# Kernel tuning notes

Measured on AMD Instinct MI355X. Metric: run time of the kernel, lower is better.

The kernel has to match this reference:

```python
import jax, jax.numpy as jnp
import numpy as np

EPS = 1e-8
INL_TH = 2.0          # RANSAC inl_th default; oneway_transfer_error squared=True
MIN_SAMPLE = 4        # minimal_sample_size for homography
MAX_LO_ITERS = 5      # RANSAC max_lo_iters
DLT_ITERS = 5         # find_homography_dlt_iterated n_iter default
SOFT_INL_TH = 3.0     # find_homography_dlt_iterated soft_inl_th default


def normalize_points(pts):
    # pts: (B,N,2) -> normalized points + (B,3,3) transforms (kornia normalize_points)
    mean = pts.mean(axis=1, keepdims=True)                      # (B,1,2)
    scale = jnp.linalg.norm(pts - mean, axis=-1).mean(axis=-1)  # (B,)
    scale = jnp.asarray(np.sqrt(2.0), pts.dtype) / (scale + EPS)
    pts_n = (pts - mean) * scale[:, None, None]
    mx, my = mean[:, 0, 0], mean[:, 0, 1]
    z = jnp.zeros_like(scale)
    o = jnp.ones_like(scale)
    T = jnp.stack([scale, z, -scale * mx,
                   z, scale, -scale * my,
                   z, z, o], axis=-1).reshape(-1, 3, 3)
    return pts_n, T


def find_homography_dlt(p1, p2, w):
    # weighted normalized DLT: p1,p2 (B,N,2), w (B,N) -> H (B,3,3)
    B = p1.shape[0]
    p1n, T1 = normalize_points(p1)
    p2n, T2 = normalize_points(p2)
    x1, y1 = p1n[..., 0], p1n[..., 1]
    x2, y2 = p2n[..., 0], p2n[..., 1]
    o = jnp.ones_like(x1)
    z = jnp.zeros_like(x1)
    ax = jnp.stack([z, z, z, -x1, -y1, -o, y2 * x1, y2 * y1, y2], axis=-1)  # (B,N,9)
    ay = jnp.stack([x1, y1, o, z, z, z, -x2 * x1, -x2 * y1, -x2], axis=-1)  # (B,N,9)
    A = jnp.stack([ax, ay], axis=2).reshape(B, -1, 9)   # (B,2N,9), ax/ay rows interleaved
    w2 = jnp.repeat(w, 2, axis=1)                       # repeat_interleave to match rows
    AtA = jnp.einsum('bni,bn,bnj->bij', A, w2, A)       # (B,9,9)
    _, _, Vh = jnp.linalg.svd(AtA)
    H = Vh[:, -1].reshape(-1, 3, 3)                     # null vector
    H = jnp.linalg.inv(T2) @ H @ T1                     # denormalize
    return H / (H[:, 2:3, 2:3] + EPS)


def transfer_errors(H, p1, p2, squared=True):
    # oneway_transfer_error: H (B,3,3), p1,p2 (N,2) -> (B,N)
    p1h = jnp.concatenate([p1, jnp.ones_like(p1[..., :1])], axis=-1)  # (N,3)
    proj = jnp.einsum('bij,nj->bni', H, p1h)                          # (B,N,3)
    zc = proj[..., 2:3]
    s = jnp.where(jnp.abs(zc) > EPS, 1.0 / zc, jnp.ones_like(zc))
    pt = proj[..., :2] * s
    err = ((pt - p2) ** 2).sum(-1)
    return err if squared else jnp.sqrt(jnp.maximum(err, 0.0))


def sample_is_valid_for_homography(p1, p2):
    # orientation-consistency of 4-point minimal samples: (B,4,2) -> (B,)
    trip = jnp.array([[0, 1, 2], [0, 2, 3], [0, 1, 3], [1, 2, 3]])
    p1h = jnp.concatenate([p1, jnp.ones_like(p1[..., :1])], axis=-1)
    p2h = jnp.concatenate([p2, jnp.ones_like(p2[..., :1])], axis=-1)
    d1 = jnp.linalg.det(p1h[:, trip])  # (B,4) triple-product signs
    d2 = jnp.linalg.det(p2h[:, trip])
    return jnp.all(jnp.sign(d1) == jnp.sign(d2), axis=1)


def polish_model(kp1, kp2, inl_mask):
    # find_homography_dlt_iterated; inlier subset expressed as zero/one weights
    w = inl_mask.astype(kp1.dtype)[None]  # (1,N)
    p1, p2 = kp1[None], kp2[None]
    H = find_homography_dlt(p1, p2, w)
    for _ in range(DLT_ITERS - 1):
        err = transfer_errors(H, kp1, kp2, squared=False)
        w_new = jnp.exp(-err / (2.0 * SOFT_INL_TH ** 2))
        H = find_homography_dlt(p1, p2, w * w_new)
    return H


def ransac_forward(kp1, kp2, idxs):
    dtype = kp1.dtype
    N = kp1.shape[0]
    kp1s, kp2s = kp1[idxs], kp2[idxs]  # (B,4,2) minimal samples
    valid_sample = sample_is_valid_for_homography(kp1s, kp2s)  # remove_bad_samples (as score mask)
    w = jnp.ones(kp1s.shape[:2], dtype)
    models = find_homography_dlt(kp1s, kp2s, w)                # (B,3,3)
    diag_min = jnp.abs(jnp.diagonal(models, axis1=1, axis2=2)).min(axis=1)
    valid_model = diag_min > 1e-4                              # remove_bad_models (as score mask)
    errors = transfer_errors(models, kp1, kp2)                 # (B,N) verify
    inl = errors <= INL_TH
    scores = inl.astype(dtype).sum(axis=1)
    scores = jnp.where(valid_sample & valid_model, scores, jnp.asarray(-1.0, dtype))
    best = jnp.argmax(scores)
    model, inliers, score = models[best], inl[best], scores[best]
    accept = score > float(MIN_SAMPLE)  # best_score_total init = minimal_sample_size

    def lo_body(carry, _):
        m, il, sc = carry
        m_lo = polish_model(kp1, kp2, il)           # (1,3,3)
        err_lo = transfer_errors(m_lo, kp1, kp2)[0]
        il_lo = err_lo <= INL_TH
        sc_lo = il_lo.astype(dtype).sum()
        better = sc_lo > sc                         # non-improving step is a fixed point == break
        m = jnp.where(better, m_lo[0], m)
        il = jnp.where(better, il_lo, il)
        sc = jnp.where(better, sc_lo, sc)
        return (m, il, sc), None

    (model, inliers, score), _ = jax.lax.scan(lo_body, (model, inliers, score), None, length=MAX_LO_ITERS)
    best_model = jnp.where(accept, model, jnp.zeros((3, 3), dtype))
    best_inliers = jnp.where(accept, inliers, jnp.zeros((N,), bool))
    return best_model, best_inliers


def setup_inputs():
    key = jax.random.key(0)
    k1, k2, k3, k4, k5 = jax.random.split(key, 5)
    N, B = 10000, 2048
    kp1 = jax.random.uniform(k1, (N, 2), jnp.float32) * 1000.0
    H_gt = jnp.array([[1.02, 0.01, 10.0], [-0.02, 0.98, -5.0], [1e-5, -1e-5, 1.0]], jnp.float32)
    p1h = jnp.concatenate([kp1, jnp.ones((N, 1), jnp.float32)], axis=-1)
    proj = p1h @ H_gt.T
    proj = proj[:, :2] / proj[:, 2:3]
    noise = jax.random.normal(k2, (N, 2), jnp.float32) * 0.5
    outliers = jax.random.uniform(k3, (N, 2), jnp.float32) * 1000.0
    is_out = jax.random.uniform(k4, (N,)) < 0.5
    kp2 = jnp.where(is_out[:, None], outliers, proj + noise)
    # minimal-sample indices without replacement (torch: rand.topk(k=4, dim=1))
    rand = jax.random.uniform(k5, (B, N))
    _, idxs = jax.lax.top_k(rand, 4)
    return {"kp1": kp1, "kp2": kp2, "idxs": idxs}


def reference(kp1, kp2, idxs):
    return ransac_forward(kp1, kp2, idxs)
```

## Files before the change

### kernel.cpp

```cpp
#include <hip/hip_runtime.h>
#include <math.h>


struct Hdr {
  int best_idx;
  float best_score;
  int pad0, pad1;
  double nrm[6];
};

__device__ __forceinline__ float sq_err9(const float h[9], float x1, float y1,
                                         float x2, float y2) {
  float px = h[0] * x1 + h[1] * y1 + h[2];
  float py = h[3] * x1 + h[4] * y1 + h[5];
  float pz = h[6] * x1 + h[7] * y1 + h[8];
  float s  = (fabsf(pz) > 1e-8f) ? (1.0f / pz) : 1.0f;
  float dx = px * s - x2;
  float dy = py * s - y2;
  return dx * dx + dy * dy;
}

__device__ __forceinline__ constexpr int TIDX(int i, int j) {
  return i * 9 - i * (i - 1) / 2 + (j - i);
}

__device__ __forceinline__ void accum_packed_f32(float* ata, float w, float x1,
                                                 float y1, float x2, float y2) {
  const int ia[6] = {3, 4, 5, 6, 7, 8};
  const int ib[6] = {0, 1, 2, 6, 7, 8};
  float va[6] = {-x1, -y1, -1.0f, x1 * y2, y1 * y2, y2};
  float vb[6] = {x1, y1, 1.0f, -x1 * x2, -y1 * x2, -x2};
#pragma unroll
  for (int u = 0; u < 6; u++) {
    float wa = w * va[u];
#pragma unroll
    for (int v = u; v < 6; v++) ata[TIDX(ia[u], ia[v])] += wa * va[v];
  }
#pragma unroll
  for (int u = 0; u < 6; u++) {
    float wb = w * vb[u];
#pragma unroll
    for (int v = u; v < 6; v++) ata[TIDX(ib[u], ib[v])] += wb * vb[v];
  }
}

__device__ __forceinline__ void accum_full_f64(double M[9][9], double x1,
                                               double y1, double x2, double y2) {
  const int ia[6] = {3, 4, 5, 6, 7, 8};
  const int ib[6] = {0, 1, 2, 6, 7, 8};
  double va[6] = {-x1, -y1, -1.0, x1 * y2, y1 * y2, y2};
  double vb[6] = {x1, y1, 1.0, -x1 * x2, -y1 * x2, -x2};
#pragma unroll
  for (int u = 0; u < 6; u++)
#pragma unroll
    for (int v = u; v < 6; v++) M[ia[u]][ia[v]] += va[u] * va[v];
#pragma unroll
  for (int u = 0; u < 6; u++)
#pragma unroll
    for (int v = u; v < 6; v++) M[ib[u]][ib[v]] += vb[u] * vb[v];
}

__device__ __forceinline__ void solve_null9(double M[9][9], double h[9]) {
  double tr = 0.0;
#pragma unroll
  for (int i = 0; i < 9; i++) {
    tr += M[i][i];
#pragma unroll
    for (int j = i + 1; j < 9; j++) M[j][i] = M[i][j];
  }
  double ridge = tr * 1e-12 + 1e-30;
#pragma unroll
  for (int i = 0; i < 9; i++) M[i][i] += ridge;
#pragma unroll
  for (int j = 0; j < 9; j++) {
    double d = M[j][j];
#pragma unroll
    for (int k = 0; k < j; k++) d -= M[j][k] * M[j][k];
    d = (d > 1e-280) ? d : 1e-280;
    double dj = sqrt(d);
    M[j][j] = dj;
    double inv = 1.0 / dj;
#pragma unroll
    for (int i = j + 1; i < 9; i++) {
      double v = M[i][j];
#pragma unroll
      for (int k = 0; k < j; k++) v -= M[i][k] * M[j][k];
      M[i][j] = v * inv;
    }
  }
  double x[9] = {1, 1, 1, 1, 1, 1, 1, 1, 1};
#pragma unroll
  for (int it = 0; it < 3; ++it) {
#pragma unroll
    for (int i = 0; i < 9; i++) {
      double v = x[i];
#pragma unroll
      for (int k = 0; k < i; k++) v -= M[i][k] * x[k];
      x[i] = v / M[i][i];
    }
#pragma unroll
    for (int i = 8; i >= 0; i--) {
      double v = x[i];
#pragma unroll
      for (int k = i + 1; k < 9; k++) v -= M[k][i] * x[k];
      x[i] = v / M[i][i];
    }
    double mx = fabs(x[0]);
#pragma unroll
    for (int i = 1; i < 9; i++) mx = fmax(mx, fabs(x[i]));
    double r = 1.0 / mx;
#pragma unroll
    for (int i = 0; i < 9; i++) x[i] *= r;
  }
#pragma unroll
  for (int i = 0; i < 9; i++) h[i] = x[i];
}

__device__ __forceinline__ void denorm9(const double hh[9], double mx1,
                                        double my1, double s1, double mx2,
                                        double my2, double s2, float out[9]) {
  double is2 = 1.0 / s2;
  double g0 = is2 * hh[0] + mx2 * hh[6];
  double g1 = is2 * hh[1] + mx2 * hh[7];
  double g2 = is2 * hh[2] + mx2 * hh[8];
  double g3 = is2 * hh[3] + my2 * hh[6];
  double g4 = is2 * hh[4] + my2 * hh[7];
  double g5 = is2 * hh[5] + my2 * hh[8];
  double g6 = hh[6], g7 = hh[7], g8 = hh[8];
  double a = -s1 * mx1, b = -s1 * my1;
  double H0 = s1 * g0, H1 = s1 * g1, H2 = a * g0 + b * g1 + g2;
  double H3 = s1 * g3, H4 = s1 * g4, H5 = a * g3 + b * g4 + g5;
  double H6 = s1 * g6, H7 = s1 * g7, H8 = a * g6 + b * g7 + g8;
  double inv = 1.0 / (H8 + 1e-8);
  out[0] = (float)(H0 * inv);
  out[1] = (float)(H1 * inv);
  out[2] = (float)(H2 * inv);
  out[3] = (float)(H3 * inv);
  out[4] = (float)(H4 * inv);
  out[5] = (float)(H5 * inv);
  out[6] = (float)(H6 * inv);
  out[7] = (float)(H7 * inv);
  out[8] = (float)(H8 * inv);
}

__global__ __launch_bounds__(256, 2) void k_fit_score(
    const float2* __restrict__ kp1, const float2* __restrict__ kp2,
    const int* __restrict__ idxs, int N, float* __restrict__ models,
    float* __restrict__ scores) {
  __shared__ float sH[9];
  __shared__ int sValid;
  __shared__ int sCnt[4];
  const int b = blockIdx.x;
  const int t = threadIdx.x;

  if (t == 0) {
    double X1[4], Y1[4], X2[4], Y2[4];
#pragma unroll
    for (int k = 0; k < 4; k++) {
      int id = idxs[b * 4 + k];
      float2 a = kp1[id];
      float2 c = kp2[id];
      X1[k] = a.x; Y1[k] = a.y; X2[k] = c.x; Y2[k] = c.y;
    }
    const int t0[4] = {0, 0, 0, 1};
    const int t1[4] = {1, 2, 1, 2};
    const int t2[4] = {2, 3, 3, 3};
    bool vs = true;
#pragma unroll
    for (int q = 0; q < 4; q++) {
      int i0 = t0[q], i1 = t1[q], i2 = t2[q];
      double d1 = (X1[i1] - X1[i0]) * (Y1[i2] - Y1[i0]) -
                  (X1[i2] - X1[i0]) * (Y1[i1] - Y1[i0]);
      double d2 = (X2[i1] - X2[i0]) * (Y2[i2] - Y2[i0]) -
                  (X2[i2] - X2[i0]) * (Y2[i1] - Y2[i0]);
      int sg1 = (d1 > 0.0) ? 1 : ((d1 < 0.0) ? -1 : 0);
      int sg2 = (d2 > 0.0) ? 1 : ((d2 < 0.0) ? -1 : 0);
      vs = vs && (sg1 == sg2);
    }
    double mx1 = (X1[0] + X1[1] + X1[2] + X1[3]) * 0.25;
    double my1 = (Y1[0] + Y1[1] + Y1[2] + Y1[3]) * 0.25;
    double mx2 = (X2[0] + X2[1] + X2[2] + X2[3]) * 0.25;
    double my2 = (Y2[0] + Y2[1] + Y2[2] + Y2[3]) * 0.25;
    double n1 = 0.0, n2 = 0.0;
#pragma unroll
    for (int k = 0; k < 4; k++) {
      double dx = X1[k] - mx1, dy = Y1[k] - my1;
      n1 += sqrt(dx * dx + dy * dy);
      dx = X2[k] - mx2; dy = Y2[k] - my2;
      n2 += sqrt(dx * dx + dy * dy);
    }
    double s1 = sqrt(2.0) / (n1 * 0.25 + 1e-8);
    double s2 = sqrt(2.0) / (n2 * 0.25 + 1e-8);
    double M[9][9];
#pragma unroll
    for (int i = 0; i < 9; i++)
#pragma unroll
      for (int j = 0; j < 9; j++) M[i][j] = 0.0;
#pragma unroll
    for (int k = 0; k < 4; k++)
      accum_full_f64(M, (X1[k] - mx1) * s1, (Y1[k] - my1) * s1,
                     (X2[k] - mx2) * s2, (Y2[k] - my2) * s2);
    double hh[9];
    solve_null9(M, hh);
    float Hf[9];
    denorm9(hh, mx1, my1, s1, mx2, my2, s2, Hf);
    bool vm =
        fminf(fminf(fabsf(Hf[0]), fabsf(Hf[4])), fabsf(Hf[8])) > 1e-4f;
#pragma unroll
    for (int j = 0; j < 9; j++) sH[j] = Hf[j];
    sValid = (vs && vm) ? 1 : 0;
  }
  __syncthreads();

  float h[9];
#pragma unroll
  for (int j = 0; j < 9; j++) h[j] = sH[j];
  int cnt = 0;
  for (int i = t; i < N; i += 256) {
    float2 a = kp1[i];
    float2 c = kp2[i];
    cnt += (sq_err9(h, a.x, a.y, c.x, c.y) <= 2.0f) ? 1 : 0;
  }
#pragma unroll
  for (int off = 32; off; off >>= 1) cnt += __shfl_down(cnt, off);
  if ((t & 63) == 0) sCnt[t >> 6] = cnt;
  __syncthreads();
  if (t == 0) {
    int tot = sCnt[0] + sCnt[1] + sCnt[2] + sCnt[3];
    scores[b] = sValid ? (float)tot : -1.0f;
#pragma unroll
    for (int j = 0; j < 9; j++) models[b * 9 + j] = sH[j];
  }
}

__global__ __launch_bounds__(1024) void k_select(
    const float2* __restrict__ kp1, const float2* __restrict__ kp2, int N,
    int B, const float* __restrict__ scores, Hdr* __restrict__ hdr) {
  const int t = threadIdx.x;
  const int lane = t & 63, wid = t >> 6;
  __shared__ float rs[1024];
  __shared__ int ri[1024];

  float bs = -2.0f;
  int bi = 0x7fffffff;
  for (int i = t; i < B; i += 1024) {
    float s = scores[i];
    if (s > bs || (s == bs && i < bi)) { bs = s; bi = i; }
  }
  rs[t] = bs;
  ri[t] = bi;
  __syncthreads();
  for (int off = 512; off; off >>= 1) {
    if (t < off) {
      float s = rs[t + off];
      int i2 = ri[t + off];
      if (s > rs[t] || (s == rs[t] && i2 < ri[t])) { rs[t] = s; ri[t] = i2; }
    }
    __syncthreads();
  }
  if (t == 0) {
    hdr->best_idx = ri[0];
    hdr->best_score = rs[0];
  }

  __shared__ double red[16][4];
  __shared__ double mb[4];
  double sx1 = 0, sy1 = 0, sx2 = 0, sy2 = 0;
  for (int i = t; i < N; i += 1024) {
    float2 a = kp1[i];
    float2 c = kp2[i];
    sx1 += a.x; sy1 += a.y; sx2 += c.x; sy2 += c.y;
  }
#pragma unroll
  for (int off = 32; off; off >>= 1) {
    sx1 += __shfl_down(sx1, off);
    sy1 += __shfl_down(sy1, off);
    sx2 += __shfl_down(sx2, off);
    sy2 += __shfl_down(sy2, off);
  }
  if (lane == 0) {
    red[wid][0] = sx1; red[wid][1] = sy1; red[wid][2] = sx2; red[wid][3] = sy2;
  }
  __syncthreads();
  if (t == 0) {
    double a = 0, b2 = 0, c = 0, d = 0;
    for (int w2 = 0; w2 < 16; w2++) {
      a += red[w2][0]; b2 += red[w2][1]; c += red[w2][2]; d += red[w2][3];
    }
    mb[0] = a / N; mb[1] = b2 / N; mb[2] = c / N; mb[3] = d / N;
  }
  __syncthreads();
  double mx1 = mb[0], my1 = mb[1], mx2 = mb[2], my2 = mb[3];
  double sn1 = 0, sn2 = 0;
  for (int i = t; i < N; i += 1024) {
    float2 a = kp1[i];
    float2 c = kp2[i];
    double dx = a.x - mx1, dy = a.y - my1;
    sn1 += sqrt(dx * dx + dy * dy);
    dx = c.x - mx2; dy = c.y - my2;
    sn2 += sqrt(dx * dx + dy * dy);
  }
#pragma unroll
  for (int off = 32; off; off >>= 1) {
    sn1 += __shfl_down(sn1, off);
    sn2 += __shfl_down(sn2, off);
  }
  __syncthreads();
  if (lane == 0) { red[wid][0] = sn1; red[wid][1] = sn2; }
  __syncthreads();
  if (t == 0) {
    double a = 0, b2 = 0;
    for (int w2 = 0; w2 < 16; w2++) { a += red[w2][0]; b2 += red[w2][1]; }
    hdr->nrm[0] = mx1;
    hdr->nrm[1] = my1;
    hdr->nrm[2] = sqrt(2.0) / (a / N + 1e-8);
    hdr->nrm[3] = mx2;
    hdr->nrm[4] = my2;
    hdr->nrm[5] = sqrt(2.0) / (b2 / N + 1e-8);
  }
}

#define K3_T 512
#define PPT 20

__global__ __launch_bounds__(512) void k_lo(const float2* __restrict__ kp1,
                                            const float2* __restrict__ kp2,
                                            int N,
                                            const float* __restrict__ models,
                                            const Hdr* __restrict__ hdr,
                                            float* __restrict__ out,
                                            int out_size) {
  const int t = threadIdx.x;
  const int lane = t & 63, wid = t >> 6;
  __shared__ double sAtA[45];
  __shared__ float sWred[8][45];
  __shared__ float sHcur[9];
  __shared__ float sHpol[9];
  __shared__ float sScLo;
  __shared__ int sCnt[8];
  __shared__ double sPar[6];
  __shared__ float sAccept;

  if (t == 0) {
    int bi = hdr->best_idx;
#pragma unroll
    for (int j = 0; j < 9; j++) sHcur[j] = models[bi * 9 + j];
    sAccept = hdr->best_score;
#pragma unroll
    for (int j = 0; j < 6; j++) sPar[j] = hdr->nrm[j];
  }
  __syncthreads();
  const bool accept = sAccept > 4.0f;
  if (!accept) {
    for (int i = t; i < out_size; i += K3_T) out[i] = 0.0f;
    return;
  }
  const float mx1 = (float)sPar[0], my1 = (float)sPar[1], s1 = (float)sPar[2];
  const float mx2 = (float)sPar[3], my2 = (float)sPar[4], s2 = (float)sPar[5];

  float hc[9];
#pragma unroll
  for (int j = 0; j < 9; j++) hc[j] = sHcur[j];
  unsigned int il = 0u;
  for (int p = 0; p < PPT; p++) {
    int i = p * K3_T + t;
    if (i < N) {
      float2 a = kp1[i];
      float2 c = kp2[i];
      if (sq_err9(hc, a.x, a.y, c.x, c.y) <= 2.0f) il |= (1u << p);
    }
  }
  float sc = sAccept;

  for (int lo = 0; lo < 5; ++lo) {
    for (int j = 0; j < 5; ++j) {
      float hp[9];
      if (j > 0) {
#pragma unroll
        for (int q = 0; q < 9; q++) hp[q] = sHpol[q];
      }
      float acc[45];
#pragma unroll
      for (int k = 0; k < 45; k++) acc[k] = 0.0f;
      for (int p = 0; p < PPT; p++) {
        int i = p * K3_T + t;
        if (i < N) {
          float w = ((il >> p) & 1u) ? 1.0f : 0.0f;
          if (w != 0.0f) {
            float2 a = kp1[i];
            float2 c = kp2[i];
            if (j > 0) {
              float e = sq_err9(hp, a.x, a.y, c.x, c.y);
              w = expf(-sqrtf(fmaxf(e, 0.0f)) / 18.0f);
            }
            float xn1 = (a.x - mx1) * s1, yn1 = (a.y - my1) * s1;
            float xn2 = (c.x - mx2) * s2, yn2 = (c.y - my2) * s2;
            accum_packed_f32(acc, w, xn1, yn1, xn2, yn2);
          }
        }
      }
#pragma unroll
      for (int k = 0; k < 45; k++) {
        float v = acc[k];
#pragma unroll
        for (int off = 32; off; off >>= 1) v += __shfl_down(v, off);
        if (lane == 0) sWred[wid][k] = v;
      }
      __syncthreads();
      if (t < 45) {
        double s = 0.0;
#pragma unroll
        for (int w2 = 0; w2 < 8; w2++) s += (double)sWred[w2][t];
        sAtA[t] = s;
      }
      __syncthreads();
      if (t == 0) {
        double M[9][9];
        int k = 0;
#pragma unroll
        for (int i2 = 0; i2 < 9; i2++)
#pragma unroll
          for (int j2 = i2; j2 < 9; j2++) M[i2][j2] = sAtA[k++];
        double hh[9];
        solve_null9(M, hh);
        float ho[9];
        denorm9(hh, sPar[0], sPar[1], sPar[2], sPar[3], sPar[4], sPar[5], ho);
#pragma unroll
        for (int q = 0; q < 9; q++) sHpol[q] = ho[q];
      }
      __syncthreads();
    }
    float hl[9];
#pragma unroll
    for (int q = 0; q < 9; q++) hl[q] = sHpol[q];
    unsigned int il_lo = 0u;
    int cnt = 0;
    for (int p = 0; p < PPT; p++) {
      int i = p * K3_T + t;
      if (i < N) {
        float2 a = kp1[i];
        float2 c = kp2[i];
        if (sq_err9(hl, a.x, a.y, c.x, c.y) <= 2.0f) {
          il_lo |= (1u << p);
          cnt++;
        }
      }
    }
#pragma unroll
    for (int off = 32; off; off >>= 1) cnt += __shfl_down(cnt, off);
    if (lane == 0) sCnt[wid] = cnt;
    __syncthreads();
    if (t == 0) {
      int tot = 0;
#pragma unroll
      for (int w2 = 0; w2 < 8; w2++) tot += sCnt[w2];
      sScLo = (float)tot;
    }
    __syncthreads();
    float sc_lo = sScLo;
    if (sc_lo > sc) {
      il = il_lo;
      sc = sc_lo;
      if (t == 0) {
#pragma unroll
        for (int q = 0; q < 9; q++) sHcur[q] = sHpol[q];
      }
    }
    __syncthreads();
  }

  if (t < 9 && t < out_size) out[t] = sHcur[t];
  for (int p = 0; p < PPT; p++) {
    int i = p * K3_T + t;
    if (i < N && (9 + i) < out_size)
      out[9 + i] = ((il >> p) & 1u) ? 1.0f : 0.0f;
  }
  for (int i = 9 + N + t; i < out_size; i += K3_T) out[i] = 0.0f;
}

extern "C" void kernel_launch(void* const* d_in, const int* in_sizes, int n_in,
                              void* d_out, int out_size, void* d_ws,
                              size_t ws_size, hipStream_t stream) {
  (void)n_in;
  (void)ws_size;
  const float2* kp1 = (const float2*)d_in[0];
  const float2* kp2 = (const float2*)d_in[1];
  const int* idxs = (const int*)d_in[2];
  const int N = in_sizes[0] / 2;
  const int B = in_sizes[2] / 4;

  float* models = (float*)d_ws;
  float* scores = models + (size_t)B * 9;
  size_t off = (((size_t)B * 10 * sizeof(float)) + 15) & ~(size_t)15;
  Hdr* hdr = (Hdr*)((char*)d_ws + off);
  float* outf = (float*)d_out;

  k_fit_score<<<B, 256, 0, stream>>>(kp1, kp2, idxs, N, models, scores);
  k_select<<<1, 1024, 0, stream>>>(kp1, kp2, N, B, scores, hdr);
  k_lo<<<1, K3_T, 0, stream>>>(kp1, kp2, N, models, hdr, outf, out_size);
}
```

Baseline: 682.3 us.

## Parallelize 9x9 null-space solve across a wavefront and restructure reductions

Replaces the single-thread Cholesky/inverse-iteration null-vector solve with a wave-parallel version where each lane holds one matrix row and uses shuffles. The fit kernel now launches one 64-thread wave per sample, builds AtA in parallel from the 8x9 design matrix, and scores with 64 threads instead of 256. The LO kernel splits the 45-entry accumulator into two 21-entry blocks and reduces through shared memory in double instead of 45 shuffle reductions. The cost targeted is the serial single-thread solve latency, which is paid in every fit block and inside the LO loop; in exchange the scoring loop has fewer threads per block and the LO kernel uses a large shared buffer.

```diff
diff --git a/kernel.cpp b/kernel.cpp
--- a/kernel.cpp
+++ b/kernel.cpp
@@ -8,6 +8,10 @@
   int pad0, pad1;
   double nrm[6];
 };
+
+__device__ __host__ constexpr int TRI6(int u, int v) {
+  return u * 6 - u * (u - 1) / 2 + (v - u);
+}
 
 __device__ __forceinline__ float sq_err9(const float h[9], float x1, float y1,
                                          float x2, float y2) {
@@ -20,100 +24,86 @@
   return dx * dx + dy * dy;
 }
 
-__device__ __forceinline__ constexpr int TIDX(int i, int j) {
-  return i * 9 - i * (i - 1) / 2 + (j - i);
-}
-
-__device__ __forceinline__ void accum_packed_f32(float* ata, float w, float x1,
-                                                 float y1, float x2, float y2) {
-  const int ia[6] = {3, 4, 5, 6, 7, 8};
-  const int ib[6] = {0, 1, 2, 6, 7, 8};
-  float va[6] = {-x1, -y1, -1.0f, x1 * y2, y1 * y2, y2};
-  float vb[6] = {x1, y1, 1.0f, -x1 * x2, -y1 * x2, -x2};
-#pragma unroll
-  for (int u = 0; u < 6; u++) {
-    float wa = w * va[u];
-#pragma unroll
-    for (int v = u; v < 6; v++) ata[TIDX(ia[u], ia[v])] += wa * va[v];
-  }
-#pragma unroll
-  for (int u = 0; u < 6; u++) {
-    float wb = w * vb[u];
-#pragma unroll
-    for (int v = u; v < 6; v++) ata[TIDX(ib[u], ib[v])] += wb * vb[v];
-  }
-}
-
-__device__ __forceinline__ void accum_full_f64(double M[9][9], double x1,
-                                               double y1, double x2, double y2) {
-  const int ia[6] = {3, 4, 5, 6, 7, 8};
-  const int ib[6] = {0, 1, 2, 6, 7, 8};
-  double va[6] = {-x1, -y1, -1.0, x1 * y2, y1 * y2, y2};
-  double vb[6] = {x1, y1, 1.0, -x1 * x2, -y1 * x2, -x2};
-#pragma unroll
-  for (int u = 0; u < 6; u++)
-#pragma unroll
-    for (int v = u; v < 6; v++) M[ia[u]][ia[v]] += va[u] * va[v];
-#pragma unroll
-  for (int u = 0; u < 6; u++)
-#pragma unroll
-    for (int v = u; v < 6; v++) M[ib[u]][ib[v]] += vb[u] * vb[v];
-}
-
-__device__ __forceinline__ void solve_null9(double M[9][9], double h[9]) {
-  double tr = 0.0;
-#pragma unroll
-  for (int i = 0; i < 9; i++) {
-    tr += M[i][i];
-#pragma unroll
-    for (int j = i + 1; j < 9; j++) M[j][i] = M[i][j];
-  }
+__device__ __forceinline__ double sel9d(const double* a, int k) {
+  double d = a[0];
+  d = (k == 1) ? a[1] : d;
+  d = (k == 2) ? a[2] : d;
+  d = (k == 3) ? a[3] : d;
+  d = (k == 4) ? a[4] : d;
+  d = (k == 5) ? a[5] : d;
+  d = (k == 6) ? a[6] : d;
+  d = (k == 7) ? a[7] : d;
+  d = (k == 8) ? a[8] : d;
+  return d;
+}
+__device__ __forceinline__ double sel4d(const double* a, int k) {
+  double d = a[0];
+  d = (k == 1) ? a[1] : d;
+  d = (k == 2) ? a[2] : d;
+  d = (k == 3) ? a[3] : d;
+  return d;
+}
+
+__device__ __forceinline__ void wave_solve9(double r[9], int lane, double* xs) {
+  double dself = sel9d(r, lane);
+  double tr = (lane < 9) ? dself : 0.0;
+#pragma unroll
+  for (int m = 1; m <= 8; m <<= 1) tr += __shfl_xor(tr, m);
   double ridge = tr * 1e-12 + 1e-30;
 #pragma unroll
-  for (int i = 0; i < 9; i++) M[i][i] += ridge;
+  for (int k = 0; k < 9; k++)
+    if (lane == k) r[k] += ridge;
+
+  double u[9];
+#pragma unroll
+  for (int k = 0; k < 9; k++) u[k] = 0.0;
+  double invd = 0.0;
+
 #pragma unroll
   for (int j = 0; j < 9; j++) {
-    double d = M[j][j];
-#pragma unroll
-    for (int k = 0; k < j; k++) d -= M[j][k] * M[j][k];
-    d = (d > 1e-280) ? d : 1e-280;
-    double dj = sqrt(d);
-    M[j][j] = dj;
-    double inv = 1.0 / dj;
-#pragma unroll
-    for (int i = j + 1; i < 9; i++) {
-      double v = M[i][j];
-#pragma unroll
-      for (int k = 0; k < j; k++) v -= M[i][k] * M[j][k];
-      M[i][j] = v * inv;
-    }
-  }
-  double x[9] = {1, 1, 1, 1, 1, 1, 1, 1, 1};
+    double dj = __shfl(r[j], j);
+    dj = (dj > 1e-280) ? dj : 1e-280;
+    double is = rsqrt(dj);
+    double s = dj * is;
+    double Lij = r[j] * is;
+    if (lane == j) { Lij = s; invd = is; }
+    r[j] = Lij;
+    double c[9];
+#pragma unroll
+    for (int k = j; k < 9; k++) c[k] = __shfl(r[j], k);
+#pragma unroll
+    for (int k = j; k < 9; k++)
+      if (lane == j) u[k] = c[k];
+    if (lane > j) {
+#pragma unroll
+      for (int k = j + 1; k < 9; k++) r[k] -= Lij * c[k];
+    }
+  }
+
+  double x = 1.0;
 #pragma unroll
   for (int it = 0; it < 3; ++it) {
-#pragma unroll
-    for (int i = 0; i < 9; i++) {
-      double v = x[i];
-#pragma unroll
-      for (int k = 0; k < i; k++) v -= M[i][k] * x[k];
-      x[i] = v / M[i][i];
-    }
-#pragma unroll
-    for (int i = 8; i >= 0; i--) {
-      double v = x[i];
-#pragma unroll
-      for (int k = i + 1; k < 9; k++) v -= M[k][i] * x[k];
-      x[i] = v / M[i][i];
-    }
-    double mx = fabs(x[0]);
-#pragma unroll
-    for (int i = 1; i < 9; i++) mx = fmax(mx, fabs(x[i]));
-    double r = 1.0 / mx;
-#pragma unroll
-    for (int i = 0; i < 9; i++) x[i] *= r;
-  }
-#pragma unroll
-  for (int i = 0; i < 9; i++) h[i] = x[i];
+    double acc = x;
+    double y = 0.0;
+#pragma unroll
+    for (int k = 0; k < 9; k++) {
+      double yk = __shfl(acc * invd, k);
+      if (lane == k) y = yk;
+      if (lane > k) acc -= r[k] * yk;
+    }
+    acc = y;
+#pragma unroll
+    for (int k = 8; k >= 0; k--) {
+      double xk = __shfl(acc * invd, k);
+      if (lane == k) x = xk;
+      if (lane < k) acc -= u[k] * xk;
+    }
+    double m2 = (lane < 9) ? fabs(x) : 0.0;
+#pragma unroll
+    for (int m = 1; m <= 8; m <<= 1) m2 = fmax(m2, __shfl_xor(m2, m));
+    x *= 1.0 / m2;
+  }
+  *xs = x;
 }
 
 __device__ __forceinline__ void denorm9(const double hh[9], double mx1,
@@ -143,72 +133,113 @@
   out[8] = (float)(H8 * inv);
 }
 
-__global__ __launch_bounds__(256, 2) void k_fit_score(
+__device__ __forceinline__ double m_entry(const double* CA, const double* CB,
+                                          int i, int j) {
+  double s = 0.0;
+  if (i >= 3) s += CA[TRI6(i - 3, j - 3)];
+  if ((i < 3 || i >= 6) && (j < 3 || j >= 6)) {
+    int ui = (i < 3) ? i : i - 3;
+    int vj = (j < 3) ? j : j - 3;
+    s += CB[TRI6(ui, vj)];
+  }
+  return s;
+}
+
+__global__ __launch_bounds__(64, 2) void k_fit_score(
     const float2* __restrict__ kp1, const float2* __restrict__ kp2,
     const int* __restrict__ idxs, int N, float* __restrict__ models,
     float* __restrict__ scores) {
+  __shared__ double sA8[8 * 9];
   __shared__ float sH[9];
-  __shared__ int sValid;
-  __shared__ int sCnt[4];
   const int b = blockIdx.x;
-  const int t = threadIdx.x;
-
-  if (t == 0) {
-    double X1[4], Y1[4], X2[4], Y2[4];
-#pragma unroll
-    for (int k = 0; k < 4; k++) {
-      int id = idxs[b * 4 + k];
-      float2 a = kp1[id];
-      float2 c = kp2[id];
-      X1[k] = a.x; Y1[k] = a.y; X2[k] = c.x; Y2[k] = c.y;
-    }
-    const int t0[4] = {0, 0, 0, 1};
-    const int t1[4] = {1, 2, 1, 2};
-    const int t2[4] = {2, 3, 3, 3};
-    bool vs = true;
-#pragma unroll
-    for (int q = 0; q < 4; q++) {
-      int i0 = t0[q], i1 = t1[q], i2 = t2[q];
-      double d1 = (X1[i1] - X1[i0]) * (Y1[i2] - Y1[i0]) -
-                  (X1[i2] - X1[i0]) * (Y1[i1] - Y1[i0]);
-      double d2 = (X2[i1] - X2[i0]) * (Y2[i2] - Y2[i0]) -
-                  (X2[i2] - X2[i0]) * (Y2[i1] - Y2[i0]);
-      int sg1 = (d1 > 0.0) ? 1 : ((d1 < 0.0) ? -1 : 0);
-      int sg2 = (d2 > 0.0) ? 1 : ((d2 < 0.0) ? -1 : 0);
-      vs = vs && (sg1 == sg2);
-    }
-    double mx1 = (X1[0] + X1[1] + X1[2] + X1[3]) * 0.25;
-    double my1 = (Y1[0] + Y1[1] + Y1[2] + Y1[3]) * 0.25;
-    double mx2 = (X2[0] + X2[1] + X2[2] + X2[3]) * 0.25;
-    double my2 = (Y2[0] + Y2[1] + Y2[2] + Y2[3]) * 0.25;
-    double n1 = 0.0, n2 = 0.0;
-#pragma unroll
-    for (int k = 0; k < 4; k++) {
-      double dx = X1[k] - mx1, dy = Y1[k] - my1;
-      n1 += sqrt(dx * dx + dy * dy);
-      dx = X2[k] - mx2; dy = Y2[k] - my2;
-      n2 += sqrt(dx * dx + dy * dy);
-    }
-    double s1 = sqrt(2.0) / (n1 * 0.25 + 1e-8);
-    double s2 = sqrt(2.0) / (n2 * 0.25 + 1e-8);
-    double M[9][9];
-#pragma unroll
-    for (int i = 0; i < 9; i++)
-#pragma unroll
-      for (int j = 0; j < 9; j++) M[i][j] = 0.0;
-#pragma unroll
-    for (int k = 0; k < 4; k++)
-      accum_full_f64(M, (X1[k] - mx1) * s1, (Y1[k] - my1) * s1,
-                     (X2[k] - mx2) * s2, (Y2[k] - my2) * s2);
-    double hh[9];
-    solve_null9(M, hh);
+  const int lane = threadIdx.x;
+
+  double X1[4], Y1[4], X2[4], Y2[4];
+#pragma unroll
+  for (int k = 0; k < 4; k++) {
+    int id = idxs[b * 4 + k];
+    float2 a = kp1[id];
+    float2 c = kp2[id];
+    X1[k] = a.x; Y1[k] = a.y; X2[k] = c.x; Y2[k] = c.y;
+  }
+  const int t0[4] = {0, 0, 0, 1};
+  const int t1[4] = {1, 2, 1, 2};
+  const int t2[4] = {2, 3, 3, 3};
+  bool vs = true;
+#pragma unroll
+  for (int q = 0; q < 4; q++) {
+    int i0 = t0[q], i1 = t1[q], i2 = t2[q];
+    double d1 = (X1[i1] - X1[i0]) * (Y1[i2] - Y1[i0]) -
+                (X1[i2] - X1[i0]) * (Y1[i1] - Y1[i0]);
+    double d2 = (X2[i1] - X2[i0]) * (Y2[i2] - Y2[i0]) -
+                (X2[i2] - X2[i0]) * (Y2[i1] - Y2[i0]);
+    int sg1 = (d1 > 0.0) ? 1 : ((d1 < 0.0) ? -1 : 0);
+    int sg2 = (d2 > 0.0) ? 1 : ((d2 < 0.0) ? -1 : 0);
+    vs = vs && (sg1 == sg2);
+  }
+  double mx1 = (X1[0] + X1[1] + X1[2] + X1[3]) * 0.25;
+  double my1 = (Y1[0] + Y1[1] + Y1[2] + Y1[3]) * 0.25;
+  double mx2 = (X2[0] + X2[1] + X2[2] + X2[3]) * 0.25;
+  double my2 = (Y2[0] + Y2[1] + Y2[2] + Y2[3]) * 0.25;
+  double n1 = 0.0, n2 = 0.0;
+#pragma unroll
+  for (int k = 0; k < 4; k++) {
+    double dx = X1[k] - mx1, dy = Y1[k] - my1;
+    n1 += sqrt(dx * dx + dy * dy);
+    dx = X2[k] - mx2; dy = Y2[k] - my2;
+    n2 += sqrt(dx * dx + dy * dy);
+  }
+  double s1 = sqrt(2.0) / (n1 * 0.25 + 1e-8);
+  double s2 = sqrt(2.0) / (n2 * 0.25 + 1e-8);
+
+  if (lane < 8) {
+    int k = lane >> 1;
+    double xn1 = (sel4d(X1, k) - mx1) * s1;
+    double yn1 = (sel4d(Y1, k) - my1) * s1;
+    double xn2 = (sel4d(X2, k) - mx2) * s2;
+    double yn2 = (sel4d(Y2, k) - my2) * s2;
+    bool odd = (lane & 1) != 0;
+    sA8[lane * 9 + 0] = odd ? xn1 : 0.0;
+    sA8[lane * 9 + 1] = odd ? yn1 : 0.0;
+    sA8[lane * 9 + 2] = odd ? 1.0 : 0.0;
+    sA8[lane * 9 + 3] = odd ? 0.0 : -xn1;
+    sA8[lane * 9 + 4] = odd ? 0.0 : -yn1;
+    sA8[lane * 9 + 5] = odd ? 0.0 : -1.0;
+    sA8[lane * 9 + 6] = odd ? -xn2 * xn1 : yn2 * xn1;
+    sA8[lane * 9 + 7] = odd ? -xn2 * yn1 : yn2 * yn1;
+    sA8[lane * 9 + 8] = odd ? -xn2 : yn2;
+  }
+  __syncthreads();
+
+  double r[9];
+  {
+    int i = (lane < 9) ? lane : 0;
+    double ai[8];
+#pragma unroll
+    for (int l = 0; l < 8; l++) ai[l] = sA8[l * 9 + i];
+#pragma unroll
+    for (int j = 0; j < 9; j++) {
+      double s = 0.0;
+#pragma unroll
+      for (int l = 0; l < 8; l++) s += ai[l] * sA8[l * 9 + j];
+      r[j] = s;
+    }
+  }
+  double xs;
+  wave_solve9(r, lane, &xs);
+
+  double hh[9];
+#pragma unroll
+  for (int k = 0; k < 9; k++) hh[k] = __shfl(xs, k);
+
+  bool valid = vs;
+  if (lane == 0) {
     float Hf[9];
     denorm9(hh, mx1, my1, s1, mx2, my2, s2, Hf);
-    bool vm =
-        fminf(fminf(fabsf(Hf[0]), fabsf(Hf[4])), fabsf(Hf[8])) > 1e-4f;
+    bool vm = fminf(fminf(fabsf(Hf[0]), fabsf(Hf[4])), fabsf(Hf[8])) > 1e-4f;
+    valid = vs && vm;
 #pragma unroll
     for (int j = 0; j < 9; j++) sH[j] = Hf[j];
-    sValid = (vs && vm) ? 1 : 0;
   }
   __syncthreads();
 
@@ -216,18 +247,15 @@
 #pragma unroll
   for (int j = 0; j < 9; j++) h[j] = sH[j];
   int cnt = 0;
-  for (int i = t; i < N; i += 256) {
+  for (int i = lane; i < N; i += 64) {
     float2 a = kp1[i];
     float2 c = kp2[i];
     cnt += (sq_err9(h, a.x, a.y, c.x, c.y) <= 2.0f) ? 1 : 0;
   }
 #pragma unroll
   for (int off = 32; off; off >>= 1) cnt += __shfl_down(cnt, off);
-  if ((t & 63) == 0) sCnt[t >> 6] = cnt;
-  __syncthreads();
-  if (t == 0) {
-    int tot = sCnt[0] + sCnt[1] + sCnt[2] + sCnt[3];
-    scores[b] = sValid ? (float)tot : -1.0f;
+  if (lane == 0) {
+    scores[b] = valid ? (float)cnt : -1.0f;
 #pragma unroll
     for (int j = 0; j < 9; j++) models[b * 9 + j] = sH[j];
   }
@@ -323,17 +351,18 @@
 #define K3_T 512
 #define PPT 20
 
-__global__ __launch_bounds__(512) void k_lo(const float2* __restrict__ kp1,
-                                            const float2* __restrict__ kp2,
-                                            int N,
-                                            const float* __restrict__ models,
-                                            const Hdr* __restrict__ hdr,
-                                            float* __restrict__ out,
-                                            int out_size) {
+__global__ __launch_bounds__(512, 2) void k_lo(const float2* __restrict__ kp1,
+                                               const float2* __restrict__ kp2,
+                                               int N,
+                                               const float* __restrict__ models,
+                                               const Hdr* __restrict__ hdr,
+                                               float* __restrict__ out,
+                                               int out_size) {
   const int t = threadIdx.x;
   const int lane = t & 63, wid = t >> 6;
-  __shared__ double sAtA[45];
-  __shared__ float sWred[8][45];
+  __shared__ float sP[K3_T * 42];
+  __shared__ double sP2[42 * 8];
+  __shared__ double sC[42];
   __shared__ float sHcur[9];
   __shared__ float sHpol[9];
   __shared__ float sScLo;
@@ -379,54 +408,78 @@
 #pragma unroll
         for (int q = 0; q < 9; q++) hp[q] = sHpol[q];
       }
-      float acc[45];
-#pragma unroll
-      for (int k = 0; k < 45; k++) acc[k] = 0.0f;
+      float accA[21], accB[21];
+#pragma unroll
+      for (int k = 0; k < 21; k++) { accA[k] = 0.0f; accB[k] = 0.0f; }
       for (int p = 0; p < PPT; p++) {
         int i = p * K3_T + t;
-        if (i < N) {
-          float w = ((il >> p) & 1u) ? 1.0f : 0.0f;
-          if (w != 0.0f) {
-            float2 a = kp1[i];
-            float2 c = kp2[i];
-            if (j > 0) {
-              float e = sq_err9(hp, a.x, a.y, c.x, c.y);
-              w = expf(-sqrtf(fmaxf(e, 0.0f)) / 18.0f);
-            }
-            float xn1 = (a.x - mx1) * s1, yn1 = (a.y - my1) * s1;
-            float xn2 = (c.x - mx2) * s2, yn2 = (c.y - my2) * s2;
-            accum_packed_f32(acc, w, xn1, yn1, xn2, yn2);
+        if (i < N && ((il >> p) & 1u)) {
+          float2 a = kp1[i];
+          float2 c = kp2[i];
+          float w = 1.0f;
+          if (j > 0) {
+            float e = sq_err9(hp, a.x, a.y, c.x, c.y);
+            w = expf(-sqrtf(fmaxf(e, 0.0f)) / 18.0f);
+          }
+          float xn1 = (a.x - mx1) * s1, yn1 = (a.y - my1) * s1;
+          float xn2 = (c.x - mx2) * s2, yn2 = (c.y - my2) * s2;
+          float va[6] = {-xn1, -yn1, -1.0f, xn1 * yn2, yn1 * yn2, yn2};
+          float vb[6] = {xn1, yn1, 1.0f, -xn1 * xn2, -yn1 * xn2, -xn2};
+#pragma unroll
+          for (int u = 0; u < 6; u++) {
+            float wa = w * va[u];
+#pragma unroll
+            for (int v = u; v < 6; v++) accA[TRI6(u, v)] += wa * va[v];
+          }
+#pragma unroll
+          for (int u = 0; u < 6; u++) {
+            float wb = w * vb[u];
+#pragma unroll
+            for (int v = u; v < 6; v++) accB[TRI6(u, v)] += wb * vb[v];
           }
         }
       }
 #pragma unroll
-      for (int k = 0; k < 45; k++) {
-        float v = acc[k];
-#pragma unroll
-        for (int off = 32; off; off >>= 1) v += __shfl_down(v, off);
-        if (lane == 0) sWred[wid][k] = v;
-      }
+      for (int k = 0; k < 21; k++) sP[t * 42 + k] = accA[k];
+#pragma unroll
+      for (int k = 0; k < 21; k++) sP[t * 42 + 21 + k] = accB[k];
       __syncthreads();
-      if (t < 45) {
+      if (t < 336) {
+        int col = t % 42, grp = t / 42;
         double s = 0.0;
-#pragma unroll
-        for (int w2 = 0; w2 < 8; w2++) s += (double)sWred[w2][t];
-        sAtA[t] = s;
+        int base = grp * 64 * 42 + col;
+        for (int i2 = 0; i2 < 64; i2++) s += (double)sP[base + i2 * 42];
+        sP2[col * 8 + grp] = s;
       }
       __syncthreads();
-      if (t == 0) {
-        double M[9][9];
-        int k = 0;
-#pragma unroll
-        for (int i2 = 0; i2 < 9; i2++)
-#pragma unroll
-          for (int j2 = i2; j2 < 9; j2++) M[i2][j2] = sAtA[k++];
+      if (t < 42) {
+        double s = 0.0;
+#pragma unroll
+        for (int g = 0; g < 8; g++) s += sP2[t * 8 + g];
+        sC[t] = s;
+      }
+      __syncthreads();
+      if (wid == 0) {
+        double r[9];
+        int i = (lane < 9) ? lane : 0;
+#pragma unroll
+        for (int jj = 0; jj < 9; jj++) {
+          int a2 = (i < jj) ? i : jj;
+          int b2 = (i < jj) ? jj : i;
+          r[jj] = m_entry(sC, sC + 21, a2, b2);
+        }
+        double xs;
+        wave_solve9(r, lane, &xs);
         double hh[9];
-        solve_null9(M, hh);
-        float ho[9];
-        denorm9(hh, sPar[0], sPar[1], sPar[2], sPar[3], sPar[4], sPar[5], ho);
-#pragma unroll
-        for (int q = 0; q < 9; q++) sHpol[q] = ho[q];
+#pragma unroll
+        for (int k = 0; k < 9; k++) hh[k] = __shfl(xs, k);
+        if (lane == 0) {
+          float ho[9];
+          denorm9(hh, sPar[0], sPar[1], sPar[2], sPar[3], sPar[4], sPar[5],
+                  ho);
+#pragma unroll
+          for (int q = 0; q < 9; q++) sHpol[q] = ho[q];
+        }
       }
       __syncthreads();
     }
@@ -495,7 +548,7 @@
   Hdr* hdr = (Hdr*)((char*)d_ws + off);
   float* outf = (float*)d_out;
 
-  k_fit_score<<<B, 256, 0, stream>>>(kp1, kp2, idxs, N, models, scores);
+  k_fit_score<<<B, 64, 0, stream>>>(kp1, kp2, idxs, N, models, scores);
   k_select<<<1, 1024, 0, stream>>>(kp1, kp2, N, B, scores, hdr);
   k_lo<<<1, K3_T, 0, stream>>>(kp1, kp2, N, models, hdr, outf, out_size);
 }
```

New measurement: 644.2 us. 1.06x faster.
